# Kernel tuning notes

Measured on AMD Instinct MI355X. Metric: run time of the kernel, lower is better.

## Reference

```python
import jax, jax.numpy as jnp
import numpy as np

B, S, HID = 2, 2048, 3584
NH, NKV, HD = 16, 8, 256
WINDOW = 1024
SOFTCAP = 50.0


def setup_inputs() -> dict:
    key = jax.random.key(0)
    ks = jax.random.split(key, 8)
    hidden_states = jax.random.normal(ks[0], (B, S, HID), dtype=jnp.float32)
    attention_mask = jnp.ones((B, S), dtype=bool)
    position_ids = jnp.tile(jnp.arange(S, dtype=jnp.int32), (B, 1))
    # rotary tables indexed by position, last dim = head_dim
    inv_freq = 1.0 / (10000.0 ** (jnp.arange(0, HD, 2, dtype=jnp.float32) / HD))
    t = jnp.arange(S, dtype=jnp.float32)
    freqs = jnp.outer(t, inv_freq)  # [S, HD/2]
    emb = jnp.concatenate([freqs, freqs], axis=-1)  # [S, HD]
    sin, cos = jnp.sin(emb), jnp.cos(emb)
    causal_mask = jnp.tril(jnp.ones((1, 1, S, S), dtype=bool))
    sc = 0.02
    Wq = jax.random.normal(ks[1], (HID, NH * HD), dtype=jnp.float32) * sc
    Wk = jax.random.normal(ks[2], (HID, NKV * HD), dtype=jnp.float32) * sc
    Wv = jax.random.normal(ks[3], (HID, NKV * HD), dtype=jnp.float32) * sc
    Wo = jax.random.normal(ks[4], (NH * HD, HID), dtype=jnp.float32) * sc
    return {"hidden_states": hidden_states, "attention_mask": attention_mask,
            "position_ids": position_ids, "sin": sin, "cos": cos,
            "causal_mask": causal_mask, "Wq": Wq, "Wk": Wk, "Wv": Wv, "Wo": Wo}


def _rotate_half(x):
    x1, x2 = x[..., : x.shape[-1] // 2], x[..., x.shape[-1] // 2 :]
    return jnp.concatenate((-x2, x1), axis=-1)


def reference(hidden_states, attention_mask, position_ids, sin, cos, causal_mask, Wq, Wk, Wv, Wo):
    b, s, _ = hidden_states.shape
    q = (hidden_states @ Wq).reshape(b, s, NH, HD)
    k = (hidden_states @ Wk).reshape(b, s, NKV, HD)
    v = (hidden_states @ Wv).reshape(b, s, NKV, HD)

    # RoPE, applied in [b, h, s, d] layout as in the original
    s_ = sin[position_ids][:, None, :, :]  # [b,1,s,d]
    c_ = cos[position_ids][:, None, :, :]
    qh = q.transpose(0, 2, 1, 3)
    kh = k.transpose(0, 2, 1, 3)
    qh = qh * c_ + _rotate_half(qh) * s_
    kh = kh * c_ + _rotate_half(kh) * s_
    q = qh.transpose(0, 2, 1, 3)  # [b,s,nh,d]
    k = kh.transpose(0, 2, 1, 3)  # [b,s,nkv,d]

    # GQA: repeat kv heads to match query heads
    groups = NH // NKV
    k = jnp.repeat(k, groups, axis=2)  # [b,s,nh,d]
    v = jnp.repeat(v, groups, axis=2)

    # combine causal + padding masks, then sliding-window (even layer)
    mask = causal_mask[:, :, :s, :s] & attention_mask[:, None, None, :]  # [b,1,s,s]
    mask = jnp.broadcast_to(mask, (b, 1, s, s))
    far_past = jnp.tril(jnp.ones((s, s), dtype=bool), k=-WINDOW)[None, None]
    mask = mask & ~far_past

    neg = jnp.finfo(jnp.float32).min
    bias = jnp.where(mask, 0.0, neg).astype(jnp.float32)

    scale = HD ** -0.5
    logits = jnp.einsum("bqhd,bkhd->bhqk", q, k) * scale
    # Gemma2 logit softcapping
    logits = SOFTCAP * jnp.tanh(logits / SOFTCAP)
    logits = logits + bias
    probs = jax.nn.softmax(logits, axis=-1)
    out = jnp.einsum("bhqk,bkhd->bqhd", probs, v)
    out = out.reshape(b, s, NH * HD)
    return out @ Wo
```

## Files before the change

kernel.cpp:

```cpp
#include <hip/hip_runtime.h>
#include <hip/hip_bf16.h>

typedef __bf16 bf16x8_t __attribute__((ext_vector_type(8)));
typedef __bf16 bf16x4_t __attribute__((ext_vector_type(4)));
typedef short s16x4_t  __attribute__((ext_vector_type(4)));
typedef float f32x4_t  __attribute__((ext_vector_type(4)));

#define NB 2
#define NS 2048
#define NHID 3584
#define NHEADS 16
#define NKVH 8
#define DH 256
#define WIN 1024

__device__ __forceinline__ float bf2f(ushort u) {
  union { unsigned v; float f; } x; x.v = ((unsigned)u) << 16; return x.f;
}
__device__ __forceinline__ ushort f2bf(float f) {
  unsigned x = __builtin_bit_cast(unsigned, f);
  unsigned r = (x + 0x7fffu + ((x >> 16) & 1u)) >> 16;
  return (ushort)r;
}

__device__ __forceinline__ void gload16(const void* g, void* l) {
  __builtin_amdgcn_global_load_lds((const __attribute__((address_space(1))) void*)g,
                                   (__attribute__((address_space(3))) void*)l, 16, 0, 0);
}

__device__ __forceinline__ f32x4_t mfma_pv(s16x4_t a, s16x4_t b, f32x4_t c) {
#if __has_builtin(__builtin_amdgcn_mfma_f32_16x16x16_bf16)
  return __builtin_amdgcn_mfma_f32_16x16x16_bf16(
      __builtin_bit_cast(bf16x4_t, a), __builtin_bit_cast(bf16x4_t, b), c, 0, 0, 0);
#else
  return __builtin_amdgcn_mfma_f32_16x16x16bf16_1k(a, b, c, 0, 0, 0);
#endif
}

__device__ __forceinline__ float fexp2(float x) {
#if __has_builtin(__builtin_amdgcn_exp2f)
  return __builtin_amdgcn_exp2f(x);
#else
  return exp2f(x);
#endif
}
__device__ __forceinline__ float frcp(float x) {
#if __has_builtin(__builtin_amdgcn_rcpf)
  return __builtin_amdgcn_rcpf(x);
#else
  return 1.0f / x;
#endif
}

__device__ __forceinline__ float pexp(float s) {
  float e = fexp2(s * 0.0036067376f);
  float r = frcp(e + 1.0f);
  return fexp2(36.067376f - 144.2695041f * r);
}

__global__ __launch_bounds__(256) void f32_to_bf16_kernel(const float* __restrict__ in,
                                                          ushort* __restrict__ out, int n4) {
  int i = (int)blockIdx.x * 256 + (int)threadIdx.x;
  if (i < n4) {
    float4 v = ((const float4*)in)[i];
    ushort4 o;
    o.x = f2bf(v.x); o.y = f2bf(v.y); o.z = f2bf(v.z); o.w = f2bf(v.w);
    ((ushort4*)out)[i] = o;
  }
}

__global__ __launch_bounds__(256) void transpose_f32_bf16(const float* __restrict__ in,
                                                          ushort* __restrict__ out,
                                                          int R, int Cc) {
  __shared__ ushort tile[64][72];
  const int t = threadIdx.x;
  const int ct = Cc >> 6;
  const int by = blockIdx.x / ct;
  const int bx = blockIdx.x % ct;
  const int r0 = by << 6, c0 = bx << 6;
#pragma unroll
  for (int i = 0; i < 4; ++i) {
    int v = i * 256 + t;
    int r = v >> 4, c4 = (v & 15) << 2;
    float4 f = *(const float4*)(in + (size_t)(r0 + r) * Cc + c0 + c4);
    ushort4 o;
    o.x = f2bf(f.x); o.y = f2bf(f.y); o.z = f2bf(f.z); o.w = f2bf(f.w);
    *(ushort4*)&tile[r][c4] = o;
  }
  __syncthreads();
#pragma unroll
  for (int i = 0; i < 2; ++i) {
    int v = i * 256 + t;
    int rr = v >> 3;
    int c8 = (v & 7) << 3;
    ushort o[8];
#pragma unroll
    for (int e = 0; e < 8; ++e) o[e] = tile[c8 + e][rr];
    *(uint4*)(out + (size_t)(c0 + rr) * R + r0 + c8) = *(const uint4*)o;
  }
}

#define TBAR do { \
    asm volatile("s_waitcnt vmcnt(0)" ::: "memory"); \
    __builtin_amdgcn_sched_barrier(0); \
    __builtin_amdgcn_s_barrier(); } while (0)

template <int EPI>
__global__ __launch_bounds__(512, 2) void gemm256(const ushort* __restrict__ A,
                                                  const ushort* __restrict__ Bt,
                                                  void* __restrict__ Cout,
                                                  const float* __restrict__ sinT,
                                                  const float* __restrict__ cosT,
                                                  int M, int N, int K) {
  __shared__ alignas(16) char lds[131072];
  const int t = threadIdx.x;
  const int lane = t & 63;
  const int wid = t >> 6;
  const int wm = wid >> 2;
  const int wn = wid & 3;
  const int g = lane >> 4;
  const int lr = lane & 15;
  const int lrow8 = lane >> 3;
  const int lp = (lane & 7) ^ lrow8;

  const int nbn = N >> 8;
  const int nwg = (int)gridDim.x;
  const int bid = (int)blockIdx.x;
  const int swz = (bid & 7) * (nwg >> 3) + (bid >> 3);
  const int bm = swz / nbn, bn = swz % nbn;
  const int m0 = bm << 8, n0 = bn << 8;

  f32x4_t acc[8][4] = {};
  const int T = K >> 6;

  auto stageA = [&](int q, int koff, int bufn) {
    int row = (q << 6) + (wid << 3) + lrow8;
    gload16(A + (size_t)(m0 + row) * K + koff + (lp << 3),
            lds + bufn * 32768 + (q << 13) + (wid << 10));
  };
  auto stageB = [&](int q, int koff, int bufn) {
    int row = (q << 6) + (wid << 3) + lrow8;
    gload16(Bt + (size_t)(n0 + row) * K + koff + (lp << 3),
            lds + 65536 + bufn * 32768 + (q << 13) + (wid << 10));
  };
  auto ldAfrag = [&](bf16x8_t* dst, const char* cA, int mh, int ks) {
#pragma unroll
    for (int i = 0; i < 4; ++i) {
      int row = (wm << 7) + (mh << 6) + (i << 4) + lr;
      dst[i] = *(const bf16x8_t*)(cA + (row << 7) + (((ks << 6) + (g << 4)) ^ ((row & 7) << 4)));
    }
  };
  auto ldBfrag = [&](bf16x8_t* dst, const char* cB, int ks) {
#pragma unroll
    for (int j = 0; j < 4; ++j) {
      int row = (wn << 6) + (j << 4) + lr;
      dst[j] = *(const bf16x8_t*)(cB + (row << 7) + (((ks << 6) + (g << 4)) ^ ((row & 7) << 4)));
    }
  };

#pragma unroll
  for (int q = 0; q < 4; ++q) { stageA(q, 0, 0); stageB(q, 0, 0); }
  asm volatile("s_waitcnt vmcnt(0)" ::: "memory");
  __builtin_amdgcn_s_barrier();

  bf16x8_t afA[4], afB[4], bfvA[4], bfvB[4];
  ldAfrag(afA, lds, 0, 0);
  ldBfrag(bfvA, lds + 65536, 0);

  for (int tt = 0; tt < T; ++tt) {
    const int bc = tt & 1;
    const int bnx = bc ^ 1;
    const bool st = (tt + 1 < T);
    const int kn = (tt + 1) << 6;
    const char* cA = lds + bc * 32768;
    const char* cB = lds + 65536 + bc * 32768;

    ldAfrag(afB, cA, 1, 0);
    if (st) { stageA(0, kn, bnx); stageA(1, kn, bnx); stageA(2, kn, bnx); stageA(3, kn, bnx); }
    __builtin_amdgcn_s_setprio(1);
#pragma unroll
    for (int i = 0; i < 4; ++i)
#pragma unroll
      for (int j = 0; j < 4; ++j)
        acc[i][j] = __builtin_amdgcn_mfma_f32_16x16x32_bf16(afA[i], bfvA[j], acc[i][j], 0, 0, 0);
    __builtin_amdgcn_s_setprio(0);

    ldAfrag(afA, cA, 0, 1);
    ldBfrag(bfvB, cB, 1);
    if (st) { stageB(0, kn, bnx); stageB(1, kn, bnx); stageB(2, kn, bnx); stageB(3, kn, bnx); }
    __builtin_amdgcn_s_setprio(1);
#pragma unroll
    for (int i = 0; i < 4; ++i)
#pragma unroll
      for (int j = 0; j < 4; ++j)
        acc[4 + i][j] = __builtin_amdgcn_mfma_f32_16x16x32_bf16(afB[i], bfvA[j], acc[4 + i][j], 0, 0, 0);
    __builtin_amdgcn_s_setprio(0);

    ldAfrag(afB, cA, 1, 1);
    __builtin_amdgcn_s_setprio(1);
#pragma unroll
    for (int i = 0; i < 4; ++i)
#pragma unroll
      for (int j = 0; j < 4; ++j)
        acc[i][j] = __builtin_amdgcn_mfma_f32_16x16x32_bf16(afA[i], bfvB[j], acc[i][j], 0, 0, 0);
    __builtin_amdgcn_s_setprio(0);

    __builtin_amdgcn_s_setprio(1);
#pragma unroll
    for (int i = 0; i < 4; ++i)
#pragma unroll
      for (int j = 0; j < 4; ++j)
        acc[4 + i][j] = __builtin_amdgcn_mfma_f32_16x16x32_bf16(afB[i], bfvB[j], acc[4 + i][j], 0, 0, 0);
    __builtin_amdgcn_s_setprio(0);
    TBAR;
    if (st) {
      ldAfrag(afA, lds + bnx * 32768, 0, 0);
      ldBfrag(bfvA, lds + 65536 + bnx * 32768, 0);
    }
  }

  __syncthreads();
  const bool trstage = (EPI == 5) && (n0 >= 2048);
  if (trstage) {
#pragma unroll
    for (int i = 0; i < 8; ++i)
#pragma unroll
      for (int j = 0; j < 4; ++j) {
        int col = (wn << 6) + (j << 4) + lr;
#pragma unroll
        for (int r = 0; r < 4; ++r) {
          int row = (wm << 7) + (i << 4) + (g << 2) + r;
          *(ushort*)(lds + (col << 9) + ((row << 1) ^ ((col & 7) << 4))) = f2bf(acc[i][j][r]);
        }
      }
  } else {
#pragma unroll
    for (int i = 0; i < 8; ++i)
#pragma unroll
      for (int j = 0; j < 4; ++j) {
        int col = (wn << 6) + (j << 4) + lr;
#pragma unroll
        for (int r = 0; r < 4; ++r) {
          int row = (wm << 7) + (i << 4) + (g << 2) + r;
          *(ushort*)(lds + (row << 9) + ((col << 1) ^ ((row & 7) << 4))) = f2bf(acc[i][j][r]);
        }
      }
  }
  __syncthreads();

  if (EPI == 1) {
    ushort* C = (ushort*)Cout;
#pragma unroll
    for (int it = 0; it < 16; ++it) {
      int idx = it * 512 + t;
      int row = idx >> 5, ch = idx & 31;
      uint4 v = *(const uint4*)(lds + (row << 9) + ((ch << 4) ^ ((row & 7) << 4)));
      uint4 p = *(const uint4*)(lds + (row << 9) + (((ch ^ 16) << 4) ^ ((row & 7) << 4)));
      int pos = (m0 + row) & (NS - 1);
      int d0 = ch << 3;
      float4 c0 = *(const float4*)(cosT + (size_t)pos * 256 + d0);
      float4 c1 = *(const float4*)(cosT + (size_t)pos * 256 + d0 + 4);
      float4 s0 = *(const float4*)(sinT + (size_t)pos * 256 + d0);
      float4 s1 = *(const float4*)(sinT + (size_t)pos * 256 + d0 + 4);
      float cs[8] = {c0.x, c0.y, c0.z, c0.w, c1.x, c1.y, c1.z, c1.w};
      float ss[8] = {s0.x, s0.y, s0.z, s0.w, s1.x, s1.y, s1.z, s1.w};
      const float sgn = (ch < 16) ? -1.f : 1.f;
      const ushort* vv = (const ushort*)&v;
      const ushort* pp = (const ushort*)&p;
      ushort o[8];
#pragma unroll
      for (int e = 0; e < 8; ++e)
        o[e] = f2bf(bf2f(vv[e]) * cs[e] + sgn * bf2f(pp[e]) * ss[e]);
      *(uint4*)(C + (size_t)(m0 + row) * N + n0 + (ch << 3)) = *(const uint4*)o;
    }
  } else if (EPI == 5) {
    ushort* C = (ushort*)Cout;
    if (n0 < 2048) {
#pragma unroll
      for (int it = 0; it < 16; ++it) {
        int idx = it * 512 + t;
        int row = idx >> 5, ch = idx & 31;
        uint4 v = *(const uint4*)(lds + (row << 9) + ((ch << 4) ^ ((row & 7) << 4)));
        uint4 p = *(const uint4*)(lds + (row << 9) + (((ch ^ 16) << 4) ^ ((row & 7) << 4)));
        int pos = (m0 + row) & (NS - 1);
        int d0 = ch << 3;
        float4 c0 = *(const float4*)(cosT + (size_t)pos * 256 + d0);
        float4 c1 = *(const float4*)(cosT + (size_t)pos * 256 + d0 + 4);
        float4 s0 = *(const float4*)(sinT + (size_t)pos * 256 + d0);
        float4 s1 = *(const float4*)(sinT + (size_t)pos * 256 + d0 + 4);
        float cs[8] = {c0.x, c0.y, c0.z, c0.w, c1.x, c1.y, c1.z, c1.w};
        float ss[8] = {s0.x, s0.y, s0.z, s0.w, s1.x, s1.y, s1.z, s1.w};
        const float sgn = (ch < 16) ? -1.f : 1.f;
        const ushort* vv = (const ushort*)&v;
        const ushort* pp = (const ushort*)&p;
        ushort o[8];
#pragma unroll
        for (int e = 0; e < 8; ++e)
          o[e] = f2bf(bf2f(vv[e]) * cs[e] + sgn * bf2f(pp[e]) * ss[e]);
        *(uint4*)(C + (size_t)(m0 + row) * 2048 + n0 + (ch << 3)) = *(const uint4*)o;
      }
    } else {
      ushort* vC = C + (size_t)4096 * 2048;
      const int plane = (m0 >> 11) * NKVH + ((n0 - 2048) >> 8);
      ushort* dst = vC + (size_t)plane * ((size_t)NS * DH) + (size_t)((m0 & (NS - 1)) >> 5) * 8192;
#pragma unroll
      for (int it = 0; it < 16; ++it) {
        int s = it * 512 + t;
        int lr2 = s & 7, kq = (s >> 3) & 7, dt_l = (s >> 6) & 15, sb_l = s >> 10;
        int d0 = (dt_l << 4) + (lr2 << 1);
        int r0 = (sb_l << 5) + (kq << 2);
        uint2 a = *(const uint2*)(lds + (d0 << 9) + ((r0 << 1) ^ ((d0 & 7) << 4)));
        uint2 b2 = *(const uint2*)(lds + ((d0 + 1) << 9) + ((r0 << 1) ^ (((d0 + 1) & 7) << 4)));
        uint4 v; v.x = a.x; v.y = a.y; v.z = b2.x; v.w = b2.y;
        *(uint4*)(dst + (size_t)s * 8) = v;
      }
    }
  } else {
    float* Cf = (float*)Cout;
#pragma unroll
    for (int it = 0; it < 32; ++it) {
      int idx = it * 512 + t;
      int row = idx >> 6, qd = idx & 63;
      ushort4 hv = *(const ushort4*)(lds + (row << 9) + ((qd << 3) ^ ((row & 7) << 4)));
      float4 fv;
      fv.x = bf2f(hv.x); fv.y = bf2f(hv.y); fv.z = bf2f(hv.z); fv.w = bf2f(hv.w);
      *(float4*)(Cf + (size_t)(m0 + row) * N + n0 + (qd << 2)) = fv;
    }
  }
}

__global__ __launch_bounds__(256) void attn_kernel(const ushort* __restrict__ q,
                                                   const ushort* __restrict__ k,
                                                   const ushort* __restrict__ vt,
                                                   ushort* __restrict__ ao) {
  __shared__ alignas(16) char lK[2][16384];
  __shared__ alignas(16) char lV[2][16384];
  const int bid = (int)blockIdx.x;
  const int x = bid & 7;
  const int s_ = bid >> 3;
  const int rnd = s_ >> 5;
  const int c = s_ & 31;
  const int a = c >> 1;
  const int hl = c & 1;
  const int plane = (x << 1) | (rnd & 1);
  int qb;
  if (rnd < 2) qb = 16 + a;
  else if (rnd == 2) qb = a;
  else qb = 15 - a;
  const int b = plane >> 3;
  const int kvh = plane & 7;
  const int h = (kvh << 1) | hl;
  const int qb0 = qb << 6;
  const int t = threadIdx.x;
  const int lane = t & 63;
  const int w = t >> 6;
  const int g = lane >> 4;
  const int lr = lane & 15;

  const int qrow = qb0 + (w << 4) + lr;
  bf16x8_t qf[8];
  const ushort* qbase = q + (size_t)(b * NS + qrow) * (NHEADS * DH) + h * DH;
#pragma unroll
  for (int ks = 0; ks < 8; ++ks)
    qf[ks] = *(const bf16x8_t*)(qbase + (ks << 5) + (g << 3));

  float l_r = 0.f;
  f32x4_t oacc[16] = {};

  const int qminw = qb0 + (w << 4);
  const int qmaxw = qminw + 15;
  int t_lo = qb0 - (WIN - 1);
  if (t_lo < 0) t_lo = 0;
  t_lo &= ~31;
  const int t_hi = qb0 + 63;
  const int nt = ((t_hi - t_lo) >> 5) + 1;

  const ushort* kgb = k + (size_t)(b * NS) * (NKVH * DH) + kvh * DH;
  const ushort* vgb = vt + (size_t)(b * NKVH + kvh) * ((size_t)NS * DH);

  auto stage = [&](int kt, int bi) {
    char* dk = lK[bi];
    char* dv = lV[bi];
    const int sb = kt >> 5;
#pragma unroll
    for (int j = 0; j < 4; ++j) {
      int i = (w << 2) + j;
      int row = (i << 1) + (lane >> 5);
      int ck = (lane & 31) ^ (row & 7);
      gload16(kgb + (size_t)(kt + row) * (NKVH * DH) + (ck << 3), dk + (i << 10));
      gload16(vgb + (size_t)sb * 8192 + (((i << 6) + lane) << 3), dv + (i << 10));
    }
  };

  int cur = 0;
  stage(t_lo, 0);
  __syncthreads();

  for (int i = 0; i < nt; ++i) {
    const int kt = t_lo + (i << 5);
    if (i + 1 < nt) stage(kt + 32, cur ^ 1);
    const char* lk = lK[cur];
    const char* lv = lV[cur];
#pragma unroll
    for (int sub = 0; sub < 2; ++sub) {
      const int key0 = kt + (sub << 4);
      if (key0 > qmaxw) continue;
      if (key0 + 15 < qminw - (WIN - 1)) continue;

      f32x4_t sacc = {};
      __builtin_amdgcn_s_setprio(1);
#pragma unroll
      for (int ks = 0; ks < 8; ++ks) {
        int row = (sub << 4) + lr;
        bf16x8_t kf = *(const bf16x8_t*)(lk + (((row << 9) + (ks << 6) + (g << 4)) ^ ((row & 7) << 4)));
        sacc = __builtin_amdgcn_mfma_f32_16x16x32_bf16(kf, qf[ks], sacc, 0, 0, 0);
      }
      __builtin_amdgcn_s_setprio(0);

      float pvv[4];
      const bool full = (key0 + 15 <= qminw) && (key0 >= qmaxw - (WIN - 1));
      if (full) {
#pragma unroll
        for (int r = 0; r < 4; ++r) { pvv[r] = pexp(sacc[r]); l_r += pvv[r]; }
      } else {
#pragma unroll
        for (int r = 0; r < 4; ++r) {
          int key = key0 + (g << 2) + r;
          bool ok = (key <= qrow) && (qrow - key < WIN);
          pvv[r] = ok ? pexp(sacc[r]) : 0.f;
          l_r += pvv[r];
        }
      }

      s16x4_t pa;
      pa[0] = (short)(ushort)(__builtin_bit_cast(unsigned, pvv[0]) >> 16);
      pa[1] = (short)(ushort)(__builtin_bit_cast(unsigned, pvv[1]) >> 16);
      pa[2] = (short)(ushort)(__builtin_bit_cast(unsigned, pvv[2]) >> 16);
      pa[3] = (short)(ushort)(__builtin_bit_cast(unsigned, pvv[3]) >> 16);

      const int kqoff = ((sub << 2) + g) << 7;
      __builtin_amdgcn_s_setprio(1);
#pragma unroll
      for (int dt = 0; dt < 16; ++dt) {
        s16x4_t vf = *(const s16x4_t*)(lv + (dt << 10) + kqoff + (lr << 3));
        oacc[dt] = mfma_pv(pa, vf, oacc[dt]);
      }
      __builtin_amdgcn_s_setprio(0);
    }
    __syncthreads();
    cur ^= 1;
  }

  l_r += __shfl_xor(l_r, 16);
  l_r += __shfl_xor(l_r, 32);
  float dn[4];
#pragma unroll
  for (int r = 0; r < 4; ++r)
    dn[r] = 1.0f / __shfl(l_r, (g << 2) + r);

  const int orow0 = b * NS + qb0 + (w << 4) + (g << 2);
#pragma unroll
  for (int dt = 0; dt < 16; ++dt) {
    int col = h * DH + (dt << 4) + lr;
#pragma unroll
    for (int r = 0; r < 4; ++r) {
      ao[(size_t)(orow0 + r) * (NHEADS * DH) + col] = f2bf(oacc[dt][r] * dn[r]);
    }
  }
}

extern "C" void kernel_launch(void* const* d_in, const int* in_sizes, int n_in,
                              void* d_out, int out_size, void* d_ws, size_t ws_size,
                              hipStream_t stream) {
  const float* hs   = (const float*)d_in[0];
  const float* sint = (const float*)d_in[3];
  const float* cost = (const float*)d_in[4];
  const float* Wq = (const float*)d_in[6];
  const float* Wk = (const float*)d_in[7];
  const float* Wv = (const float*)d_in[8];
  const float* Wo = (const float*)d_in[9];

  char* ws = (char*)d_ws;
  size_t off = 0;
  auto alloc = [&](size_t bytes) {
    char* p = ws + off;
    off += (bytes + 255) & ~(size_t)255;
    return p;
  };
  ushort* hsb   = (ushort*)alloc((size_t)4096 * 3584 * 2);
  ushort* wT    = (ushort*)alloc((size_t)4096 * 3584 * 2);
  ushort* qbuf  = (ushort*)alloc((size_t)4096 * 4096 * 2);
  ushort* kbuf  = (ushort*)alloc((size_t)4096 * 2048 * 2);
  ushort* vtbuf = (ushort*)alloc((size_t)4096 * 2048 * 2);
  ushort* aobuf = qbuf;
  if (off > ws_size) return;

  f32_to_bf16_kernel<<<(4096 * 3584 / 4) / 256, 256, 0, stream>>>(hs, hsb, 4096 * 3584 / 4);

  transpose_f32_bf16<<<(3584 / 64) * (2048 / 64), 256, 0, stream>>>(Wk, wT, 3584, 2048);
  transpose_f32_bf16<<<(3584 / 64) * (2048 / 64), 256, 0, stream>>>(Wv, wT + (size_t)2048 * 3584, 3584, 2048);
  gemm256<5><<<16 * 16, 512, 0, stream>>>(hsb, wT, kbuf, sint, cost, 4096, 4096, 3584);

  transpose_f32_bf16<<<(3584 / 64) * (4096 / 64), 256, 0, stream>>>(Wq, wT, 3584, 4096);
  gemm256<1><<<16 * 16, 512, 0, stream>>>(hsb, wT, qbuf, sint, cost, 4096, 4096, 3584);

  attn_kernel<<<NB * NHEADS * (NS / 64), 256, 0, stream>>>(qbuf, kbuf, vtbuf, aobuf);

  transpose_f32_bf16<<<(4096 / 64) * (3584 / 64), 256, 0, stream>>>(Wo, wT, 4096, 3584);
  gemm256<2><<<16 * 14, 512, 0, stream>>>(aobuf, wT, d_out, nullptr, nullptr, 4096, 3584, 4096);
}
```

Before: 512.3 us.

## Switch GEMM main loop to four-stage LDS ring with K-step 32

Replaces the double-buffered K=64 tile loop in the shared GEMM with a four-slot LDS ring of K=32 tiles, prefetched three tiles ahead. Waits use partial vmcnt counts so that later global loads can stay in flight while the current tile is consumed. The goal is to hide global-load latency better and drop the full vmcnt(0) wait that preceded every barrier. In exchange there are twice as many barriers per unit of K and half as many MFMAs between them. Each wave's vmcnt wait now comes after the barrier, so it only covers that wave's own loads, and data written by other waves may not be guaranteed visible.

```diff
diff --git a/kernel.cpp b/kernel.cpp
--- a/kernel.cpp
+++ b/kernel.cpp
@@ -99,11 +99,6 @@
     *(uint4*)(out + (size_t)(c0 + rr) * R + r0 + c8) = *(const uint4*)o;
   }
 }
-
-#define TBAR do { \
-    asm volatile("s_waitcnt vmcnt(0)" ::: "memory"); \
-    __builtin_amdgcn_sched_barrier(0); \
-    __builtin_amdgcn_s_barrier(); } while (0)
 
 template <int EPI>
 __global__ __launch_bounds__(512, 2) void gemm256(const ushort* __restrict__ A,
@@ -120,8 +115,6 @@
   const int wn = wid & 3;
   const int g = lane >> 4;
   const int lr = lane & 15;
-  const int lrow8 = lane >> 3;
-  const int lp = (lane & 7) ^ lrow8;
 
   const int nbn = N >> 8;
   const int nwg = (int)gridDim.x;
@@ -131,91 +124,73 @@
   const int m0 = bm << 8, n0 = bn << 8;
 
   f32x4_t acc[8][4] = {};
-  const int T = K >> 6;
-
-  auto stageA = [&](int q, int koff, int bufn) {
-    int row = (q << 6) + (wid << 3) + lrow8;
-    gload16(A + (size_t)(m0 + row) * K + koff + (lp << 3),
-            lds + bufn * 32768 + (q << 13) + (wid << 10));
+  const int T = K >> 5;
+
+  auto stageAB = [&](int tt) {
+    const int bufo = (tt & 3) << 14;
+    const int koff = tt << 5;
+#pragma unroll
+    for (int j = 0; j < 2; ++j) {
+      int idx = (j << 9) + t;
+      int row = idx >> 2;
+      int sc = (idx & 3) ^ (row & 3);
+      gload16(A + (size_t)(m0 + row) * K + koff + (sc << 3),
+              lds + bufo + (idx << 4));
+      gload16(Bt + (size_t)(n0 + row) * K + koff + (sc << 3),
+              lds + 65536 + bufo + (idx << 4));
+    }
   };
-  auto stageB = [&](int q, int koff, int bufn) {
-    int row = (q << 6) + (wid << 3) + lrow8;
-    gload16(Bt + (size_t)(n0 + row) * K + koff + (lp << 3),
-            lds + 65536 + bufn * 32768 + (q << 13) + (wid << 10));
-  };
-  auto ldAfrag = [&](bf16x8_t* dst, const char* cA, int mh, int ks) {
+  auto ldAfrag = [&](bf16x8_t* dst, int tt, int mh) {
+    const char* cA = lds + ((tt & 3) << 14);
 #pragma unroll
     for (int i = 0; i < 4; ++i) {
       int row = (wm << 7) + (mh << 6) + (i << 4) + lr;
-      dst[i] = *(const bf16x8_t*)(cA + (row << 7) + (((ks << 6) + (g << 4)) ^ ((row & 7) << 4)));
+      dst[i] = *(const bf16x8_t*)(cA + (row << 6) + ((g << 4) ^ ((row & 3) << 4)));
     }
   };
-  auto ldBfrag = [&](bf16x8_t* dst, const char* cB, int ks) {
+  auto ldBfrag = [&](bf16x8_t* dst, int tt) {
+    const char* cB = lds + 65536 + ((tt & 3) << 14);
 #pragma unroll
     for (int j = 0; j < 4; ++j) {
       int row = (wn << 6) + (j << 4) + lr;
-      dst[j] = *(const bf16x8_t*)(cB + (row << 7) + (((ks << 6) + (g << 4)) ^ ((row & 7) << 4)));
+      dst[j] = *(const bf16x8_t*)(cB + (row << 6) + ((g << 4) ^ ((row & 3) << 4)));
     }
   };
 
-#pragma unroll
-  for (int q = 0; q < 4; ++q) { stageA(q, 0, 0); stageB(q, 0, 0); }
-  asm volatile("s_waitcnt vmcnt(0)" ::: "memory");
+  stageAB(0); stageAB(1); stageAB(2);
+  asm volatile("s_waitcnt vmcnt(8)" ::: "memory");
+  __builtin_amdgcn_sched_barrier(0);
   __builtin_amdgcn_s_barrier();
 
-  bf16x8_t afA[4], afB[4], bfvA[4], bfvB[4];
-  ldAfrag(afA, lds, 0, 0);
-  ldBfrag(bfvA, lds + 65536, 0);
+  bf16x8_t afA[4], afB[4], bfv[4];
+  ldAfrag(afA, 0, 0);
+  ldBfrag(bfv, 0);
 
   for (int tt = 0; tt < T; ++tt) {
-    const int bc = tt & 1;
-    const int bnx = bc ^ 1;
-    const bool st = (tt + 1 < T);
-    const int kn = (tt + 1) << 6;
-    const char* cA = lds + bc * 32768;
-    const char* cB = lds + 65536 + bc * 32768;
-
-    ldAfrag(afB, cA, 1, 0);
-    if (st) { stageA(0, kn, bnx); stageA(1, kn, bnx); stageA(2, kn, bnx); stageA(3, kn, bnx); }
+    if (tt + 3 < T) stageAB(tt + 3);
+    ldAfrag(afB, tt, 1);
     __builtin_amdgcn_s_setprio(1);
 #pragma unroll
     for (int i = 0; i < 4; ++i)
 #pragma unroll
       for (int j = 0; j < 4; ++j)
-        acc[i][j] = __builtin_amdgcn_mfma_f32_16x16x32_bf16(afA[i], bfvA[j], acc[i][j], 0, 0, 0);
+        acc[i][j] = __builtin_amdgcn_mfma_f32_16x16x32_bf16(afA[i], bfv[j], acc[i][j], 0, 0, 0);
     __builtin_amdgcn_s_setprio(0);
-
-    ldAfrag(afA, cA, 0, 1);
-    ldBfrag(bfvB, cB, 1);
-    if (st) { stageB(0, kn, bnx); stageB(1, kn, bnx); stageB(2, kn, bnx); stageB(3, kn, bnx); }
     __builtin_amdgcn_s_setprio(1);
 #pragma unroll
     for (int i = 0; i < 4; ++i)
 #pragma unroll
       for (int j = 0; j < 4; ++j)
-        acc[4 + i][j] = __builtin_amdgcn_mfma_f32_16x16x32_bf16(afB[i], bfvA[j], acc[4 + i][j], 0, 0, 0);
+        acc[4 + i][j] = __builtin_amdgcn_mfma_f32_16x16x32_bf16(afB[i], bfv[j], acc[4 + i][j], 0, 0, 0);
     __builtin_amdgcn_s_setprio(0);
-
-    ldAfrag(afB, cA, 1, 1);
-    __builtin_amdgcn_s_setprio(1);
-#pragma unroll
-    for (int i = 0; i < 4; ++i)
-#pragma unroll
-      for (int j = 0; j < 4; ++j)
-        acc[i][j] = __builtin_amdgcn_mfma_f32_16x16x32_bf16(afA[i], bfvB[j], acc[i][j], 0, 0, 0);
-    __builtin_amdgcn_s_setprio(0);
-
-    __builtin_amdgcn_s_setprio(1);
-#pragma unroll
-    for (int i = 0; i < 4; ++i)
-#pragma unroll
-      for (int j = 0; j < 4; ++j)
-        acc[4 + i][j] = __builtin_amdgcn_mfma_f32_16x16x32_bf16(afB[i], bfvB[j], acc[4 + i][j], 0, 0, 0);
-    __builtin_amdgcn_s_setprio(0);
-    TBAR;
-    if (st) {
-      ldAfrag(afA, lds + bnx * 32768, 0, 0);
-      ldBfrag(bfvA, lds + 65536 + bnx * 32768, 0);
+    __builtin_amdgcn_s_barrier();
+    if (tt + 1 < T) {
+      if (tt + 3 < T)      asm volatile("s_waitcnt vmcnt(8)" ::: "memory");
+      else if (tt + 2 < T) asm volatile("s_waitcnt vmcnt(4)" ::: "memory");
+      else                 asm volatile("s_waitcnt vmcnt(0)" ::: "memory");
+      __builtin_amdgcn_sched_barrier(0);
+      ldAfrag(afA, tt + 1, 0);
+      ldBfrag(bfv, tt + 1);
     }
   }
 
```

Result: slower. 557.1 us (+8.8%).
